# Kernel optimization log

Measured on AMD Instinct MI355X. Metric: run time of the kernel, lower is better.

## Reference

```python
import jax, jax.numpy as jnp
import numpy as np

H, W = 256, 192           # cfg.input_img_shape
INF = 9999.0
B, V = 64, 100000


def setup_inputs() -> dict:
    key = jax.random.key(0)
    k1, k2, k3 = jax.random.split(key, 3)
    sdf = jax.random.normal(k1, (B, V), dtype=jnp.float32)
    # pixel coords spanning slightly beyond the image so some verts are invalid
    uv = jax.random.uniform(k2, (B, V, 2), dtype=jnp.float32)
    cloth_meshes = uv * jnp.array([W * 1.1, H * 1.1], jnp.float32) - jnp.array([W * 0.05, H * 0.05], jnp.float32)
    parse_gt = jax.random.randint(k3, (B, H, W), 0, 2).astype(jnp.int32)
    return {
        "sdf": sdf,
        "cloth_meshes": cloth_meshes,
        "parse_gt": parse_gt,
        "sdf_thresh": jnp.ones((1,), jnp.float32),
        "cloth_meshes_unposed": jnp.zeros((1, 1, 3), jnp.float32),
        "parse_valid": jnp.ones((B, 1, 1), jnp.float32),
        "dist_thresh": jnp.ones((1,), jnp.float32),
        "v_template": jnp.zeros((1, 3), jnp.float32),
    }


def reference(sdf, cloth_meshes, parse_gt, sdf_thresh, cloth_meshes_unposed, parse_valid, dist_thresh, v_template):
    b = sdf.shape[0]
    hw = H * W
    x = cloth_meshes[:, :, 0].astype(jnp.int32)
    y = cloth_meshes[:, :, 1].astype(jnp.int32)
    is_valid = (x >= 0) & (x < W) & (y >= 0) & (y < H)
    idx = jnp.where(is_valid, y * W + x, 0)                      # [B,V]
    min_sdf = jnp.where(is_valid, sdf, INF)
    max_sdf = jnp.where(is_valid, sdf, -INF)
    # single flattened segment reduce over B*H*W segments (scatter_min/max)
    flat_idx = (idx + jnp.arange(b, dtype=jnp.int32)[:, None] * hw).reshape(-1)
    pmin = jax.ops.segment_min(min_sdf.reshape(-1), flat_idx, num_segments=b * hw).reshape(b, H, W)
    pmax = jax.ops.segment_max(max_sdf.reshape(-1), flat_idx, num_segments=b * hw).reshape(b, H, W)
    # empty / all-invalid pixels: torch init was +/-INF -> replace
    pmin = jnp.where(pmin >= INF, 0.0, pmin)
    pmax = jnp.where(pmax <= -INF, sdf_thresh[0], pmax)
    pos_mask = (parse_gt == 1).astype(sdf.dtype)
    neg_mask = (parse_gt == 0).astype(sdf.dtype)
    loss_pos = jnp.abs(pmin) * pos_mask * parse_valid
    loss_neg = jnp.abs(pmax - sdf_thresh[0]) * neg_mask * parse_valid
    loss = loss_pos.mean((1, 2)) + loss_neg.mean((1, 2))
    cloth_exist = (pos_mask.sum((1, 2)) > 0).astype(sdf.dtype)
    return loss * cloth_exist
```

## Files before the change

### kernel.cpp

```cpp
#include <hip/hip_runtime.h>


#define HH 256
#define WW 192
#define HW (HH * WW)
#define NB 64
#define NV 100000
#define NS 4
#define RANGE (HW / NS)
#define NTHR 1024
#define G4 (NV / 4)
#define MAGIC 0x9E3779B9u

__device__ __forceinline__ unsigned fkey(float f) {
    unsigned u = __float_as_uint(f);
    return (u & 0x80000000u) ? ~u : (u | 0x80000000u);
}
__device__ __forceinline__ float funkey(unsigned k) {
    unsigned u = (k & 0x80000000u) ? (k ^ 0x80000000u) : ~k;
    return __uint_as_float(u);
}

__global__ __launch_bounds__(NTHR) void direct_kernel(
        const float4* __restrict__ sdf4,
        const float4* __restrict__ mesh4,
        const int4*   __restrict__ gt4,
        const float*  __restrict__ thr_p,
        const float*  __restrict__ pv,
        unsigned*     __restrict__ hs,
        float*        __restrict__ out) {
    __shared__ unsigned ldsk[RANGE];
    __shared__ unsigned char gtb[RANGE];
    __shared__ float    wsum[16];
    __shared__ unsigned wflag[16];
    const int b = blockIdx.x & 63;
    const int q = blockIdx.x >> 6;
    const int tid = threadIdx.x;

    int lpos = 0;
    for (int j = tid; j < RANGE; j += NTHR) ldsk[j] = 0xFFFFFFFFu;
    const int4* gbase = gt4 + ((size_t)b * HW + (size_t)q * RANGE) / 4;
    for (int j = tid; j < RANGE / 4; j += NTHR) {
        int4 g = gbase[j];
        gtb[4 * j + 0] = (unsigned char)g.x;
        gtb[4 * j + 1] = (unsigned char)g.y;
        gtb[4 * j + 2] = (unsigned char)g.z;
        gtb[4 * j + 3] = (unsigned char)g.w;
        lpos |= (g.x == 1) | (g.y == 1) | (g.z == 1) | (g.w == 1);
    }
    __syncthreads();

    const float4* sbase = sdf4  + (size_t)b * (NV / 4);
    const float4* mbase = mesh4 + (size_t)b * (NV / 2);
    const int qlo = q << 6;
    int gi = tid;
    float4 sc = sbase[gi];
    float4 mac = mbase[2 * gi];
    float4 mbc = mbase[2 * gi + 1];
    while (true) {
        const int gn = gi + NTHR;
        const bool nxt = gn < G4;
        float4 sn, man, mbn;
        if (nxt) {
            sn  = sbase[gn];
            man = mbase[2 * gn];
            mbn = mbase[2 * gn + 1];
        }
        {
            float xs[4] = {mac.x, mac.z, mbc.x, mbc.z};
            float ys[4] = {mac.y, mac.w, mbc.y, mbc.w};
            float ss[4] = {sc.x, sc.y, sc.z, sc.w};
            #pragma unroll
            for (int j = 0; j < 4; ++j) {
                int x = (int)xs[j];
                int y = (int)ys[j];
                if ((unsigned)x < WW && (unsigned)(y - qlo) < 64u) {
                    unsigned p = (unsigned)(y - qlo) * WW + (unsigned)x;
                    unsigned k = fkey(ss[j]);
                    if (gtb[p] == 0) k = ~k;
                    atomicMin(&ldsk[p], k);
                }
            }
        }
        if (!nxt) break;
        sc = sn; mac = man; mbc = mbn; gi = gn;
    }
    __syncthreads();

    const float thr = thr_p[0];
    float lsum = 0.f;
    for (int j = tid; j < RANGE; j += NTHR) {
        unsigned k = ldsk[j];
        if (k != 0xFFFFFFFFu) {
            if (gtb[j]) lsum += fabsf(funkey(k));
            else        lsum += fabsf(funkey(~k) - thr);
        }
    }
    #pragma unroll
    for (int off = 32; off > 0; off >>= 1)
        lsum += __shfl_down(lsum, off, 64);
    unsigned long long m = __ballot(lpos != 0);
    const int wid = tid >> 6;
    if ((tid & 63) == 0) { wsum[wid] = lsum; wflag[wid] = (m != 0); }
    __syncthreads();

    if (tid == 0) {
        float s = 0.f; unsigned f = 0;
        #pragma unroll
        for (int i = 0; i < NTHR / 64; ++i) { s += wsum[i]; f |= wflag[i]; }

        if (q != 0) {
            unsigned* e = hs + 4 * ((q - 1) * NB + b);
            unsigned sb = __float_as_uint(s);
            __hip_atomic_store(e + 0, sb, __ATOMIC_RELAXED,
                               __HIP_MEMORY_SCOPE_AGENT);
            __hip_atomic_store(e + 1, f, __ATOMIC_RELAXED,
                               __HIP_MEMORY_SCOPE_AGENT);
            __hip_atomic_store(e + 2, sb ^ f ^ MAGIC, __ATOMIC_RELEASE,
                               __HIP_MEMORY_SCOPE_AGENT);
        } else {
            float tot = s; unsigned fall = f;
            #pragma unroll 1
            for (int qq = 0; qq < NS - 1; ++qq) {
                const unsigned* e = hs + 4 * (qq * NB + b);
                unsigned e0, e1, e2;
                while (true) {
                    e2 = __hip_atomic_load(e + 2, __ATOMIC_ACQUIRE,
                                           __HIP_MEMORY_SCOPE_AGENT);
                    e0 = __hip_atomic_load(e + 0, __ATOMIC_RELAXED,
                                           __HIP_MEMORY_SCOPE_AGENT);
                    e1 = __hip_atomic_load(e + 1, __ATOMIC_RELAXED,
                                           __HIP_MEMORY_SCOPE_AGENT);
                    if ((e0 ^ e1 ^ MAGIC) == e2) break;
                    __builtin_amdgcn_s_sleep(2);
                }
                tot += __uint_as_float(e0);
                fall |= e1;
            }
            out[b] = fall ? tot * (1.0f / HW) * pv[b] : 0.0f;
        }
    }
}

extern "C" void kernel_launch(void* const* d_in, const int* in_sizes, int n_in,
                              void* d_out, int out_size, void* d_ws, size_t ws_size,
                              hipStream_t stream) {
    const float4* sdf4  = (const float4*)d_in[0];
    const float4* mesh4 = (const float4*)d_in[1];
    const int4*   gt4   = (const int4*)d_in[2];
    const float*  thr   = (const float*)d_in[3];
    const float*  pv    = (const float*)d_in[5];
    float* out = (float*)d_out;

    unsigned* hs = (unsigned*)d_ws;

    direct_kernel<<<NS * NB, NTHR, 0, stream>>>(
        sdf4, mesh4, gt4, thr, pv, hs, out);
}
```

Baseline: 141.6 us.

## Track min and max separately and double-buffer vertex loads two strides ahead

The scatter now keeps separate min and max LDS arrays and issues both atomicMin and atomicMax per vertex. This removes the need to stage parse_gt into LDS before the scatter, so the gt load moves into the final reduction and is read directly from global memory. The vertex loop is restructured into a fixed-count loop that processes two strides per iteration and prefetches the next two, aiming for more memory-level parallelism. The cost is twice the LDS atomics and twice the LDS footprint, which may reduce occupancy.

```diff
diff --git a/kernel.cpp b/kernel.cpp
--- a/kernel.cpp
+++ b/kernel.cpp
@@ -10,6 +10,7 @@
 #define RANGE (HW / NS)
 #define NTHR 1024
 #define G4 (NV / 4)
+#define NIT 13
 #define MAGIC 0x9E3779B9u
 
 __device__ __forceinline__ unsigned fkey(float f) {
@@ -29,71 +30,95 @@
         const float*  __restrict__ pv,
         unsigned*     __restrict__ hs,
         float*        __restrict__ out) {
-    __shared__ unsigned ldsk[RANGE];
-    __shared__ unsigned char gtb[RANGE];
+    __shared__ unsigned lmin[RANGE];
+    __shared__ unsigned lmax[RANGE];
     __shared__ float    wsum[16];
     __shared__ unsigned wflag[16];
     const int b = blockIdx.x & 63;
     const int q = blockIdx.x >> 6;
     const int tid = threadIdx.x;
 
-    int lpos = 0;
-    for (int j = tid; j < RANGE; j += NTHR) ldsk[j] = 0xFFFFFFFFu;
-    const int4* gbase = gt4 + ((size_t)b * HW + (size_t)q * RANGE) / 4;
+    uint4* lmin4 = (uint4*)lmin;
+    uint4* lmax4 = (uint4*)lmax;
     for (int j = tid; j < RANGE / 4; j += NTHR) {
-        int4 g = gbase[j];
-        gtb[4 * j + 0] = (unsigned char)g.x;
-        gtb[4 * j + 1] = (unsigned char)g.y;
-        gtb[4 * j + 2] = (unsigned char)g.z;
-        gtb[4 * j + 3] = (unsigned char)g.w;
-        lpos |= (g.x == 1) | (g.y == 1) | (g.z == 1) | (g.w == 1);
+        lmin4[j] = make_uint4(0xFFFFFFFFu, 0xFFFFFFFFu, 0xFFFFFFFFu, 0xFFFFFFFFu);
+        lmax4[j] = make_uint4(0u, 0u, 0u, 0u);
     }
     __syncthreads();
 
     const float4* sbase = sdf4  + (size_t)b * (NV / 4);
     const float4* mbase = mesh4 + (size_t)b * (NV / 2);
     const int qlo = q << 6;
+
+#define PROC(s4, ma, mb) do {                                               \
+        float xs[4] = {(ma).x, (ma).z, (mb).x, (mb).z};                     \
+        float ys[4] = {(ma).y, (ma).w, (mb).y, (mb).w};                     \
+        float ss[4] = {(s4).x, (s4).y, (s4).z, (s4).w};                     \
+        _Pragma("unroll")                                                   \
+        for (int j = 0; j < 4; ++j) {                                       \
+            int x = (int)xs[j];     \
+            int y = (int)ys[j];                                             \
+            if ((unsigned)x < WW && (unsigned)(y - qlo) < 64u) {            \
+                unsigned p = (unsigned)(y - qlo) * WW + (unsigned)x;        \
+                unsigned k = fkey(ss[j]);                                   \
+                atomicMin(&lmin[p], k);                                     \
+                atomicMax(&lmax[p], k);                                     \
+            }                                                               \
+        }                                                                   \
+    } while (0)
+
     int gi = tid;
-    float4 sc = sbase[gi];
-    float4 mac = mbase[2 * gi];
-    float4 mbc = mbase[2 * gi + 1];
-    while (true) {
-        const int gn = gi + NTHR;
-        const bool nxt = gn < G4;
-        float4 sn, man, mbn;
-        if (nxt) {
-            sn  = sbase[gn];
-            man = mbase[2 * gn];
-            mbn = mbase[2 * gn + 1];
-        }
-        {
-            float xs[4] = {mac.x, mac.z, mbc.x, mbc.z};
-            float ys[4] = {mac.y, mac.w, mbc.y, mbc.w};
-            float ss[4] = {sc.x, sc.y, sc.z, sc.w};
-            #pragma unroll
-            for (int j = 0; j < 4; ++j) {
-                int x = (int)xs[j];
-                int y = (int)ys[j];
-                if ((unsigned)x < WW && (unsigned)(y - qlo) < 64u) {
-                    unsigned p = (unsigned)(y - qlo) * WW + (unsigned)x;
-                    unsigned k = fkey(ss[j]);
-                    if (gtb[p] == 0) k = ~k;
-                    atomicMin(&ldsk[p], k);
-                }
-            }
-        }
-        if (!nxt) break;
-        sc = sn; mac = man; mbc = mbn; gi = gn;
+    float4 As0 = sbase[gi],          As1 = sbase[gi + NTHR];
+    float4 Am0 = mbase[2 * gi],      Am1 = mbase[2 * gi + 1];
+    float4 Am2 = mbase[2 * (gi + NTHR)], Am3 = mbase[2 * (gi + NTHR) + 1];
+
+    #pragma unroll 1
+    for (int it = 0; it < NIT; ++it) {
+        const int gj = gi + 2 * NTHR;
+        const int p0 = gj        < G4 ? gj        : G4 - 1;
+        const int p1 = gj + NTHR < G4 ? gj + NTHR : G4 - 1;
+        float4 Bs0 = sbase[p0],      Bs1 = sbase[p1];
+        float4 Bm0 = mbase[2 * p0],  Bm1 = mbase[2 * p0 + 1];
+        float4 Bm2 = mbase[2 * p1],  Bm3 = mbase[2 * p1 + 1];
+        asm volatile("" :: "v"(Bs0.x), "v"(Bs1.x), "v"(Bm0.x),
+                           "v"(Bm1.x), "v"(Bm2.x), "v"(Bm3.x));
+
+        if (gi < G4)        PROC(As0, Am0, Am1);
+        if (gi + NTHR < G4) PROC(As1, Am2, Am3);
+
+        As0 = Bs0; As1 = Bs1;
+        Am0 = Bm0; Am1 = Bm1; Am2 = Bm2; Am3 = Bm3;
+        gi = gj;
     }
+#undef PROC
     __syncthreads();
 
     const float thr = thr_p[0];
     float lsum = 0.f;
-    for (int j = tid; j < RANGE; j += NTHR) {
-        unsigned k = ldsk[j];
-        if (k != 0xFFFFFFFFu) {
-            if (gtb[j]) lsum += fabsf(funkey(k));
-            else        lsum += fabsf(funkey(~k) - thr);
+    int lpos = 0;
+    const int4* gbase = gt4 + ((size_t)b * HW + (size_t)q * RANGE) / 4;
+    const uint4* lm4 = (const uint4*)lmin;
+    const uint4* lx4 = (const uint4*)lmax;
+    for (int j = tid; j < RANGE / 4; j += NTHR) {
+        int4 g = gbase[j];
+        uint4 km = lm4[j];
+        uint4 kx = lx4[j];
+        lpos |= (g.x == 1) | (g.y == 1) | (g.z == 1) | (g.w == 1);
+        if (km.x != 0xFFFFFFFFu) {
+            if (g.x == 1) lsum += fabsf(funkey(km.x));
+            else          lsum += fabsf(funkey(kx.x) - thr);
+        }
+        if (km.y != 0xFFFFFFFFu) {
+            if (g.y == 1) lsum += fabsf(funkey(km.y));
+            else          lsum += fabsf(funkey(kx.y) - thr);
+        }
+        if (km.z != 0xFFFFFFFFu) {
+            if (g.z == 1) lsum += fabsf(funkey(km.z));
+            else          lsum += fabsf(funkey(kx.z) - thr);
+        }
+        if (km.w != 0xFFFFFFFFu) {
+            if (g.w == 1) lsum += fabsf(funkey(km.w));
+            else          lsum += fabsf(funkey(kx.w) - thr);
         }
     }
     #pragma unroll
```

Measured after the change: 139.7 us. About the same (-1.3%).

## Double-width software-pipelined vertex loop with batched LDS lookups and vectorized init/reduce

Applied to the files above, without the earlier changes.

Each loop iteration now processes two float4 groups (8 vertices) per thread for a fixed 13 iterations. Next-iteration loads are clamped to the last element instead of being branched, and an empty asm statement forces them to issue early. The gtb lookups are batched ahead of the LDS atomicMin calls to raise memory-level parallelism and hide global latency. LDS init and the final reduction use 128-bit vector accesses. The cost is higher register pressure, and the clamped tail re-reads the same element, which is harmless for min.

```diff
diff --git a/kernel.cpp b/kernel.cpp
--- a/kernel.cpp
+++ b/kernel.cpp
@@ -10,6 +10,7 @@
 #define RANGE (HW / NS)
 #define NTHR 1024
 #define G4 (NV / 4)
+#define NIT 13
 #define MAGIC 0x9E3779B9u
 
 __device__ __forceinline__ unsigned fkey(float f) {
@@ -37,10 +38,11 @@
     const int q = blockIdx.x >> 6;
     const int tid = threadIdx.x;
 
+    uint4* ldsk4 = (uint4*)ldsk;
     int lpos = 0;
-    for (int j = tid; j < RANGE; j += NTHR) ldsk[j] = 0xFFFFFFFFu;
     const int4* gbase = gt4 + ((size_t)b * HW + (size_t)q * RANGE) / 4;
     for (int j = tid; j < RANGE / 4; j += NTHR) {
+        ldsk4[j] = make_uint4(0xFFFFFFFFu, 0xFFFFFFFFu, 0xFFFFFFFFu, 0xFFFFFFFFu);
         int4 g = gbase[j];
         gtb[4 * j + 0] = (unsigned char)g.x;
         gtb[4 * j + 1] = (unsigned char)g.y;
@@ -53,48 +55,63 @@
     const float4* sbase = sdf4  + (size_t)b * (NV / 4);
     const float4* mbase = mesh4 + (size_t)b * (NV / 2);
     const int qlo = q << 6;
+
     int gi = tid;
-    float4 sc = sbase[gi];
-    float4 mac = mbase[2 * gi];
-    float4 mbc = mbase[2 * gi + 1];
-    while (true) {
-        const int gn = gi + NTHR;
-        const bool nxt = gn < G4;
-        float4 sn, man, mbn;
-        if (nxt) {
-            sn  = sbase[gn];
-            man = mbase[2 * gn];
-            mbn = mbase[2 * gn + 1];
+    float4 As0 = sbase[gi],              As1 = sbase[gi + NTHR];
+    float4 Am0 = mbase[2 * gi],          Am1 = mbase[2 * gi + 1];
+    float4 Am2 = mbase[2 * (gi + NTHR)], Am3 = mbase[2 * (gi + NTHR) + 1];
+
+    #pragma unroll 1
+    for (int it = 0; it < NIT; ++it) {
+        const int gj = gi + 2 * NTHR;
+        const int pA = gj        < G4 ? gj        : G4 - 1;
+        const int pB = gj + NTHR < G4 ? gj + NTHR : G4 - 1;
+        float4 Ns0 = sbase[pA],     Ns1 = sbase[pB];
+        float4 Nm0 = mbase[2 * pA], Nm1 = mbase[2 * pA + 1];
+        float4 Nm2 = mbase[2 * pB], Nm3 = mbase[2 * pB + 1];
+        asm volatile("" :: "v"(Ns0.x), "v"(Ns1.x), "v"(Nm0.x),
+                           "v"(Nm1.x), "v"(Nm2.x), "v"(Nm3.x));
+
+        float xs[8] = {Am0.x, Am0.z, Am1.x, Am1.z, Am2.x, Am2.z, Am3.x, Am3.z};
+        float ys[8] = {Am0.y, Am0.w, Am1.y, Am1.w, Am2.y, Am2.w, Am3.y, Am3.w};
+        float ss[8] = {As0.x, As0.y, As0.z, As0.w, As1.x, As1.y, As1.z, As1.w};
+        unsigned pp[8], kk[8];
+        bool vv[8];
+        #pragma unroll
+        for (int i = 0; i < 8; ++i) {
+            int x = (int)xs[i];
+            int y = (int)ys[i];
+            vv[i] = ((unsigned)x < WW) & ((unsigned)(y - qlo) < 64u);
+            pp[i] = vv[i] ? (unsigned)(y - qlo) * WW + (unsigned)x : 0u;
+            kk[i] = fkey(ss[i]);
         }
-        {
-            float xs[4] = {mac.x, mac.z, mbc.x, mbc.z};
-            float ys[4] = {mac.y, mac.w, mbc.y, mbc.w};
-            float ss[4] = {sc.x, sc.y, sc.z, sc.w};
-            #pragma unroll
-            for (int j = 0; j < 4; ++j) {
-                int x = (int)xs[j];
-                int y = (int)ys[j];
-                if ((unsigned)x < WW && (unsigned)(y - qlo) < 64u) {
-                    unsigned p = (unsigned)(y - qlo) * WW + (unsigned)x;
-                    unsigned k = fkey(ss[j]);
-                    if (gtb[p] == 0) k = ~k;
-                    atomicMin(&ldsk[p], k);
-                }
-            }
-        }
-        if (!nxt) break;
-        sc = sn; mac = man; mbc = mbn; gi = gn;
+        unsigned gb[8];
+        #pragma unroll
+        for (int i = 0; i < 8; ++i) gb[i] = gtb[pp[i]];
+        #pragma unroll
+        for (int i = 0; i < 8; ++i)
+            if (vv[i]) atomicMin(&ldsk[pp[i]], gb[i] ? kk[i] : ~kk[i]);
+
+        As0 = Ns0; As1 = Ns1;
+        Am0 = Nm0; Am1 = Nm1; Am2 = Nm2; Am3 = Nm3;
+        gi = gj;
     }
     __syncthreads();
 
     const float thr = thr_p[0];
+    const uchar4* gtb4 = (const uchar4*)gtb;
     float lsum = 0.f;
-    for (int j = tid; j < RANGE; j += NTHR) {
-        unsigned k = ldsk[j];
-        if (k != 0xFFFFFFFFu) {
-            if (gtb[j]) lsum += fabsf(funkey(k));
-            else        lsum += fabsf(funkey(~k) - thr);
-        }
+    for (int j = tid; j < RANGE / 4; j += NTHR) {
+        uint4 kq = ldsk4[j];
+        uchar4 gq = gtb4[j];
+        if (kq.x != 0xFFFFFFFFu)
+            lsum += gq.x ? fabsf(funkey(kq.x)) : fabsf(funkey(~kq.x) - thr);
+        if (kq.y != 0xFFFFFFFFu)
+            lsum += gq.y ? fabsf(funkey(kq.y)) : fabsf(funkey(~kq.y) - thr);
+        if (kq.z != 0xFFFFFFFFu)
+            lsum += gq.z ? fabsf(funkey(kq.z)) : fabsf(funkey(~kq.z) - thr);
+        if (kq.w != 0xFFFFFFFFu)
+            lsum += gq.w ? fabsf(funkey(kq.w)) : fabsf(funkey(~kq.w) - thr);
     }
     #pragma unroll
     for (int off = 32; off > 0; off >>= 1)
```

Measured after the change: 138.4 us (median of 2 runs). 1.02x faster.
